# Performance work log

Measured on AMD Instinct MI355X. Metric: run time of the kernel, lower is better.

Reference implementation:

```python
import jax, jax.numpy as jnp
import numpy as np

B, N, DIM = 64, 64, 256
HEADS, P = 4, 16
H, W, C = 56, 56, 256
CH = C // HEADS            # per-head channels = eff_in_dim = eff_out_dim = 64
IN_PTS = HEADS * P         # 64
OUT_PTS = IN_PTS           # 64
TOTAL = CH * CH + IN_PTS * OUT_PTS  # 8192
GRAD_NORM = 1.0 / H

# RestrictGradNorm: identity fwd, clamp grad in bwd
@jax.custom_vjp
def restrict_grad(x):
    return x

def _rg_fwd(x):
    return x, None

def _rg_bwd(_, g):
    return (jnp.clip(g, -GRAD_NORM, GRAD_NORM),)

restrict_grad.defvjp(_rg_fwd, _rg_bwd)


def grid_sample_bilinear(feat, grid):
    # feat [G,c,h,w], grid [G,Hg,Wg,2] in [-1,1]; align_corners=False, zeros padding
    G, c, h, w = feat.shape
    Hg, Wg = grid.shape[1], grid.shape[2]
    Q = Hg * Wg
    x = (grid[..., 0] + 1.0) * 0.5 * w - 0.5
    y = (grid[..., 1] + 1.0) * 0.5 * h - 0.5
    x0f = jnp.floor(x); y0f = jnp.floor(y)
    wx1 = x - x0f; wx0 = 1.0 - wx1
    wy1 = y - y0f; wy0 = 1.0 - wy1
    x0 = x0f.astype(jnp.int32); y0 = y0f.astype(jnp.int32)
    fflat = feat.reshape(G, c, h * w)

    def gather(xi, yi):
        valid = (xi >= 0) & (xi < w) & (yi >= 0) & (yi < h)
        idx = (jnp.clip(yi, 0, h - 1) * w + jnp.clip(xi, 0, w - 1)).reshape(G, Q)
        v = jnp.take_along_axis(fflat, jnp.broadcast_to(idx[:, None, :], (G, c, Q)), axis=2)
        return v * valid.reshape(G, 1, Q)

    out = (gather(x0, y0) * (wx0 * wy0).reshape(G, 1, Q)
           + gather(x0 + 1, y0) * (wx1 * wy0).reshape(G, 1, Q)
           + gather(x0, y0 + 1) * (wx0 * wy1).reshape(G, 1, Q)
           + gather(x0 + 1, y0 + 1) * (wx1 * wy1).reshape(G, 1, Q))
    return out.reshape(G, c, Hg, Wg)


def setup_inputs() -> dict:
    key = jax.random.key(0)
    ks = jax.random.split(key, 10)
    img_feat = jax.random.normal(ks[0], (B, C, H, W), jnp.float32)
    ctr = jax.random.uniform(ks[1], (B, N, 2), jnp.float32) * 0.8 + 0.1
    wh = jax.random.uniform(ks[2], (B, N, 2), jnp.float32) * 0.4 + 0.1
    token_roi = jnp.concatenate([ctr - wh / 2, ctr + wh / 2], axis=-1)
    query = jax.random.normal(ks[3], (B, N, DIM), jnp.float32)
    W_off = jax.random.normal(ks[4], (DIM, HEADS * P * 2), jnp.float32) * 0.02
    b_off = jnp.zeros((HEADS * P * 2,), jnp.float32)
    ln_w = jnp.ones((DIM,), jnp.float32)
    ln_b = jnp.zeros((DIM,), jnp.float32)
    W1 = jax.random.normal(ks[5], (DIM, DIM // 4), jnp.float32) * 0.02
    b1 = jnp.zeros((DIM // 4,), jnp.float32)
    W2 = jax.random.normal(ks[6], (DIM // 4, TOTAL), jnp.float32) * 0.02
    b2 = jax.random.normal(ks[7], (TOTAL,), jnp.float32) * 0.02
    m_beta = jnp.zeros((CH,), jnp.float32)
    s_beta = jnp.zeros((OUT_PTS,), jnp.float32)
    W_out = jax.random.normal(ks[8], (CH * OUT_PTS, DIM), jnp.float32) * 0.02
    b_out = jnp.zeros((DIM,), jnp.float32)
    return dict(img_feat=img_feat, token_roi=token_roi, query=query, W_off=W_off,
                b_off=b_off, ln_w=ln_w, ln_b=ln_b, W1=W1, b1=b1, W2=W2, b2=b2,
                m_beta=m_beta, s_beta=s_beta, W_out=W_out, b_out=b_out)


def _forward(img_feat, token_roi, query, W_off, b_off, ln_w, ln_b, W1, b1, W2, b2,
             m_beta, s_beta, W_out, b_out):
    # 1) sampling offsets from query
    off = (query @ W_off + b_off).reshape(B, N, 1, IN_PTS, 2)
    # 2) make_absolute_sampling_point: normalize over points (unbiased std, as torch)
    mean = off.mean(axis=-2, keepdims=True)
    std = jnp.std(off, axis=-2, ddof=1, keepdims=True) + 1e-7
    off = (off - mean) / (3.0 * std)
    roi_xy = (token_roi[:, :, 2:] + token_roi[:, :, :2]) * 0.5   # [B,N,2]
    roi_wh = token_roi[:, :, 2:] - token_roi[:, :, :2]
    pts = roi_xy[:, :, None, None, :] + off * roi_wh[:, :, None, None, :]  # [B,N,1,HP,2]
    # 3) sampling_from_img_feat: per-head bilinear grid sample
    sp = pts.reshape(B, N, 1, HEADS, P, 2).transpose(0, 3, 1, 2, 4, 5)
    sp = sp.reshape(B * HEADS, N, P, 2)
    sp = restrict_grad(sp)
    grid = sp * 2.0 - 1.0
    feat = img_feat.reshape(B * HEADS, CH, H, W)
    out = grid_sample_bilinear(feat, grid)                        # [B*HEADS, CH, N, P]
    out = out.reshape(B, HEADS, CH, N, 1, P).transpose(0, 3, 4, 1, 5, 2)
    sampled = out.reshape(B * N, IN_PTS, CH)                      # g==1 in AdaptiveMixing
    # 4) AdaptiveMixing: parameter generator (LN eps 1e-6 -> Linear -> Linear)
    mu = query.mean(-1, keepdims=True)
    var = query.var(-1, keepdims=True)
    qn = (query - mu) / jnp.sqrt(var + 1e-6) * ln_w + ln_b
    params = ((qn @ W1 + b1) @ W2 + b2).reshape(B * N, TOTAL)
    cm = params[:, :CH * CH].reshape(B * N, CH, CH)               # channel mixing
    sm = params[:, CH * CH:].reshape(B * N, OUT_PTS, IN_PTS)      # spatial mixing
    x = jax.nn.gelu(jnp.einsum('bpc,bcd->bpd', sampled, cm) + m_beta, approximate=False)
    x = jax.nn.gelu(jnp.einsum('bop,bpc->boc', sm, x) + s_beta[None, :, None], approximate=False)
    x = x.reshape(B, N, OUT_PTS * CH) @ W_out + b_out
    return x


def reference(img_feat, token_roi, query, W_off, b_off, ln_w, ln_b, W1, b1, W2, b2,
              m_beta, s_beta, W_out, b_out):
    return _forward(img_feat, token_roi, query, W_off, b_off, ln_w, ln_b, W1, b1,
                    W2, b2, m_beta, s_beta, W_out, b_out)
```

## Files before the change

### kernel.cpp

```cpp
#include <hip/hip_runtime.h>


typedef unsigned short u16;
typedef u16 u16x8 __attribute__((ext_vector_type(8)));
typedef short bf16x8 __attribute__((ext_vector_type(8)));
typedef float f32x4 __attribute__((ext_vector_type(4)));
#define SA 72
#define MFMA(a, b, c) __builtin_amdgcn_mfma_f32_16x16x32_bf16(a, b, c, 0, 0, 0)

static __device__ __forceinline__ float bf2f(u16 s) {
    union { float f; unsigned u; } v; v.u = ((unsigned)s) << 16; return v.f;
}
static __device__ __forceinline__ u16 f2bf(float f) {
    union { float f; unsigned u; } v; v.f = f;
    unsigned r = v.u + 0x7fffu + ((v.u >> 16) & 1u);
    return (u16)(r >> 16);
}
static __device__ __forceinline__ float gelu(float x) {
    return 0.5f * x * (1.0f + erff(x * 0.70710678118654752f));
}
static __device__ __forceinline__ float loadf(const void* p, size_t i, int isbf) {
    return isbf ? bf2f(((const u16*)p)[i]) : ((const float*)p)[i];
}

__global__ void kdetect(const void* __restrict__ lnw, int* __restrict__ flag) {
    if (threadIdx.x == 0) {
        unsigned v = *(const unsigned*)lnw;
        *flag = (v == 0x3F800000u) ? 0 : 1;
    }
}

__global__ void k0_transpose(const void* __restrict__ img, u16* __restrict__ featT,
                             const int* __restrict__ flag) {
    __shared__ __align__(16) float tile[64 * 65];
    const int pos0 = blockIdx.x * 64, c0 = blockIdx.y * 64, bz = blockIdx.z;
    const int tid = threadIdx.x;
    const int isbf = *flag;
#pragma unroll
    for (int i = 0; i < 16; i++) {
        int e = i * 256 + tid;
        int cy = e >> 6, px = e & 63;
        tile[cy * 65 + px] = loadf(img, ((size_t)bz * 256 + c0 + cy) * 3136 + pos0 + px, isbf);
    }
    __syncthreads();
#pragma unroll
    for (int i = 0; i < 16; i++) {
        int e = i * 256 + tid;
        int cy = e & 63, px = e >> 6;
        featT[((size_t)bz * 3136 + pos0 + px) * 256 + c0 + cy] = f2bf(tile[cy * 65 + px]);
    }
}

__global__ void k1_points(const void* __restrict__ query, const void* __restrict__ roi,
                          const void* __restrict__ W_off, const void* __restrict__ b_off,
                          const void* __restrict__ ln_w, const void* __restrict__ ln_b,
                          const void* __restrict__ W1, const void* __restrict__ b1,
                          const int* __restrict__ flag,
                          float* __restrict__ pts, u16* __restrict__ hbuf) {
    __shared__ float qf[256], qn[256], offl[128], red[4], stats[8];
    const int t = blockIdx.x, tid = threadIdx.x;
    const int isbf = *flag;
    float q = loadf(query, (size_t)t * 256 + tid, isbf);
    qf[tid] = q;
    float v = q;
#pragma unroll
    for (int o = 32; o; o >>= 1) v += __shfl_down(v, o, 64);
    if ((tid & 63) == 0) red[tid >> 6] = v;
    __syncthreads();
    if (tid == 0) stats[0] = (red[0] + red[1] + red[2] + red[3]) * (1.f / 256.f);
    __syncthreads();
    float mu = stats[0];
    float dv = q - mu;
    v = dv * dv;
#pragma unroll
    for (int o = 32; o; o >>= 1) v += __shfl_down(v, o, 64);
    if ((tid & 63) == 0) red[tid >> 6] = v;
    __syncthreads();
    if (tid == 0) stats[1] = (red[0] + red[1] + red[2] + red[3]) * (1.f / 256.f);
    __syncthreads();
    float inv = rsqrtf(stats[1] + 1e-6f);
    qn[tid] = dv * inv * loadf(ln_w, tid, isbf) + loadf(ln_b, tid, isbf);
    __syncthreads();
    if (tid < 128) {
        float a = loadf(b_off, tid, isbf);
        for (int d = 0; d < 256; d++) a = fmaf(qf[d], loadf(W_off, (size_t)d * 128 + tid, isbf), a);
        offl[tid] = a;
    } else if (tid < 192) {
        int k = tid - 128;
        float a = loadf(b1, k, isbf);
        for (int d = 0; d < 256; d++) a = fmaf(qn[d], loadf(W1, (size_t)d * 64 + k, isbf), a);
        hbuf[(size_t)t * 64 + k] = f2bf(a);
    }
    __syncthreads();
    if (tid < 2) {
        float m = 0.f;
        for (int p = 0; p < 64; p++) m += offl[p * 2 + tid];
        m *= (1.f / 64.f);
        float s2 = 0.f;
        for (int p = 0; p < 64; p++) { float d = offl[p * 2 + tid] - m; s2 += d * d; }
        float sd = sqrtf(s2 * (1.f / 63.f));
        stats[2 + tid] = m;
        stats[4 + tid] = 1.f / (3.f * (sd + 1e-7f));
    }
    __syncthreads();
    if (tid < 128) {
        int xy = tid & 1;
        float lo = loadf(roi, (size_t)t * 4 + xy, isbf);
        float hi = loadf(roi, (size_t)t * 4 + 2 + xy, isbf);
        float ctr = 0.5f * (lo + hi), wh = hi - lo;
        pts[(size_t)t * 128 + tid] = ctr + (offl[tid] - stats[2 + xy]) * stats[4 + xy] * wh;
    }
}

__global__ void k2_sample_t(const u16* __restrict__ featT, const float* __restrict__ pts,
                            u16* __restrict__ sampled) {
    const int t = blockIdx.x, tid = threadIdx.x;
    const int pt = tid >> 2, cg = tid & 3;
    const int b = t >> 6, hh = pt >> 4;
    const float px = pts[(size_t)t * 128 + pt * 2], py = pts[(size_t)t * 128 + pt * 2 + 1];
    const float x = px * 56.f - 0.5f, y = py * 56.f - 0.5f;
    const float x0f = floorf(x), y0f = floorf(y);
    const int ix0 = (int)x0f, iy0 = (int)y0f;
    const float wx1 = x - x0f, wx0 = 1.f - wx1, wy1 = y - y0f, wy0 = 1.f - wy1;
    float acc[16];
#pragma unroll
    for (int i = 0; i < 16; i++) acc[i] = 0.f;
    const int chbase = hh * 64 + cg * 16;
#pragma unroll
    for (int corner = 0; corner < 4; corner++) {
        const int xi = ix0 + (corner & 1), yi = iy0 + (corner >> 1);
        const float wgt = ((corner & 1) ? wx1 : wx0) * ((corner >> 1) ? wy1 : wy0);
        if (xi >= 0 && xi < 56 && yi >= 0 && yi < 56) {
            const u16x8* p8 = (const u16x8*)&featT[((size_t)b * 3136 + yi * 56 + xi) * 256 + chbase];
            u16x8 a = p8[0], c = p8[1];
#pragma unroll
            for (int i = 0; i < 8; i++) {
                acc[i]     = fmaf(wgt, bf2f(a[i]), acc[i]);
                acc[8 + i] = fmaf(wgt, bf2f(c[i]), acc[8 + i]);
            }
        }
    }
    u16x8 o0, o1;
#pragma unroll
    for (int i = 0; i < 8; i++) { o0[i] = f2bf(acc[i]); o1[i] = f2bf(acc[8 + i]); }
    u16x8* q8 = (u16x8*)&sampled[(size_t)t * 4096 + pt * 64 + cg * 16];
    q8[0] = o0; q8[1] = o1;
}

__global__ void k2_sample_d(const void* __restrict__ img, const float* __restrict__ pts,
                            u16* __restrict__ sampled, const int* __restrict__ flag) {
    const int t = blockIdx.x, tid = threadIdx.x;
    const int pt = tid >> 2, cg = tid & 3;
    const int b = t >> 6, hh = pt >> 4;
    const int isbf = *flag;
    const float px = pts[(size_t)t * 128 + pt * 2], py = pts[(size_t)t * 128 + pt * 2 + 1];
    const float x = px * 56.f - 0.5f, y = py * 56.f - 0.5f;
    const float x0f = floorf(x), y0f = floorf(y);
    const int ix0 = (int)x0f, iy0 = (int)y0f;
    const float wx1 = x - x0f, wx0 = 1.f - wx1, wy1 = y - y0f, wy0 = 1.f - wy1;
    float acc[16];
#pragma unroll
    for (int i = 0; i < 16; i++) acc[i] = 0.f;
    const int chbase = b * 256 + hh * 64 + cg * 16;
#pragma unroll
    for (int corner = 0; corner < 4; corner++) {
        const int xi = ix0 + (corner & 1), yi = iy0 + (corner >> 1);
        const float wgt = ((corner & 1) ? wx1 : wx0) * ((corner >> 1) ? wy1 : wy0);
        if (xi >= 0 && xi < 56 && yi >= 0 && yi < 56) {
            const size_t sp = yi * 56 + xi;
#pragma unroll
            for (int i = 0; i < 16; i++)
                acc[i] = fmaf(wgt, loadf(img, ((size_t)(chbase + i)) * 3136 + sp, isbf), acc[i]);
        }
    }
    for (int i = 0; i < 16; i++)
        sampled[(size_t)t * 4096 + pt * 64 + cg * 16 + i] = f2bf(acc[i]);
}

__global__ __launch_bounds__(256) void k4_mfma(const u16* __restrict__ hb,
        const void* __restrict__ W2, const void* __restrict__ b2,
        const int* __restrict__ flag, u16* __restrict__ params) {
    __shared__ u16 As[64 * SA];
    __shared__ u16 Bs[64 * SA];
    const int tid = threadIdx.x;
    const int m0 = blockIdx.x * 64, n0 = blockIdx.y * 64;
    const int isbf = *flag;
    const int lane = tid & 63, w = tid >> 6;
    const int wm = w & 1, wn = w >> 1;
    const int l16 = lane & 15, quad = lane >> 4;
    {
        const int row = tid >> 2, kp = (tid & 3) * 16;
        const u16x8* ga = (const u16x8*)&hb[(size_t)(m0 + row) * 64 + kp];
        *(u16x8*)&As[row * SA + kp]     = ga[0];
        *(u16x8*)&As[row * SA + kp + 8] = ga[1];
    }
    {
        const int n = tid & 63, kp = (tid >> 6) * 16;
        u16x8 b0, b1;
#pragma unroll
        for (int j = 0; j < 8; j++) {
            b0[j] = f2bf(loadf(W2, (size_t)(kp + j) * 8192 + n0 + n, isbf));
            b1[j] = f2bf(loadf(W2, (size_t)(kp + 8 + j) * 8192 + n0 + n, isbf));
        }
        *(u16x8*)&Bs[n * SA + kp]     = b0;
        *(u16x8*)&Bs[n * SA + kp + 8] = b1;
    }
    __syncthreads();
    f32x4 acc[2][2];
#pragma unroll
    for (int i = 0; i < 2; i++)
#pragma unroll
        for (int j = 0; j < 2; j++) acc[i][j] = (f32x4){0.f, 0.f, 0.f, 0.f};
#pragma unroll
    for (int kk = 0; kk < 64; kk += 32) {
        bf16x8 af[2], bf[2];
        af[0] = *(const bf16x8*)&As[(wm * 32 + l16) * SA + kk + quad * 8];
        af[1] = *(const bf16x8*)&As[(wm * 32 + 16 + l16) * SA + kk + quad * 8];
        bf[0] = *(const bf16x8*)&Bs[(wn * 32 + l16) * SA + kk + quad * 8];
        bf[1] = *(const bf16x8*)&Bs[(wn * 32 + 16 + l16) * SA + kk + quad * 8];
#pragma unroll
        for (int tm = 0; tm < 2; tm++)
#pragma unroll
            for (int tn = 0; tn < 2; tn++)
                acc[tm][tn] = MFMA(af[tm], bf[tn], acc[tm][tn]);
    }
    float bb[2];
    bb[0] = loadf(b2, n0 + wn * 32 + l16, isbf);
    bb[1] = loadf(b2, n0 + wn * 32 + 16 + l16, isbf);
#pragma unroll
    for (int tm = 0; tm < 2; tm++)
#pragma unroll
        for (int tn = 0; tn < 2; tn++)
#pragma unroll
            for (int r = 0; r < 4; r++) {
                int row = m0 + wm * 32 + tm * 16 + quad * 4 + r;
                int col = n0 + wn * 32 + tn * 16 + l16;
                params[(size_t)row * 8192 + col] = f2bf(acc[tm][tn][r] + bb[tn]);
            }
}

__global__ __launch_bounds__(256) void k5_mfma(const u16* __restrict__ params,
        const void* __restrict__ m_beta, const void* __restrict__ s_beta,
        const int* __restrict__ flag, u16* __restrict__ sampled) {
    __shared__ u16 S[64 * SA];
    __shared__ u16 CMT[64 * SA];
    __shared__ u16 SM[64 * SA];
    __shared__ u16 X1T[64 * SA];
    const int t = blockIdx.x, tid = threadIdx.x;
    const int isbf = *flag;
    const size_t pbase = (size_t)t * 8192, sbase = (size_t)t * 4096;
    const int lane = tid & 63, w = tid >> 6;
    const int wm = w & 1, wn = w >> 1;
    const int l16 = lane & 15, quad = lane >> 4;
    {
        const int r = tid >> 2, cp = (tid & 3) * 16;
        const u16x8* gs = (const u16x8*)&sampled[sbase + r * 64 + cp];
        *(u16x8*)&S[r * SA + cp]     = gs[0];
        *(u16x8*)&S[r * SA + cp + 8] = gs[1];
        const u16x8* gm = (const u16x8*)&params[pbase + 4096 + r * 64 + cp];
        *(u16x8*)&SM[r * SA + cp]     = gm[0];
        *(u16x8*)&SM[r * SA + cp + 8] = gm[1];
    }
    {
        const int d = tid & 63, cp = (tid >> 6) * 16;
        u16x8 b0, b1;
#pragma unroll
        for (int j = 0; j < 8; j++) {
            b0[j] = params[pbase + (size_t)(cp + j) * 64 + d];
            b1[j] = params[pbase + (size_t)(cp + 8 + j) * 64 + d];
        }
        *(u16x8*)&CMT[d * SA + cp]     = b0;
        *(u16x8*)&CMT[d * SA + cp + 8] = b1;
    }
    __syncthreads();
    f32x4 acc[2][2];
#pragma unroll
    for (int i = 0; i < 2; i++)
#pragma unroll
        for (int j = 0; j < 2; j++) acc[i][j] = (f32x4){0.f, 0.f, 0.f, 0.f};
#pragma unroll
    for (int kk = 0; kk < 64; kk += 32) {
        bf16x8 af[2], bf[2];
        af[0] = *(const bf16x8*)&S[(wm * 32 + l16) * SA + kk + quad * 8];
        af[1] = *(const bf16x8*)&S[(wm * 32 + 16 + l16) * SA + kk + quad * 8];
        bf[0] = *(const bf16x8*)&CMT[(wn * 32 + l16) * SA + kk + quad * 8];
        bf[1] = *(const bf16x8*)&CMT[(wn * 32 + 16 + l16) * SA + kk + quad * 8];
#pragma unroll
        for (int tm = 0; tm < 2; tm++)
#pragma unroll
            for (int tn = 0; tn < 2; tn++)
                acc[tm][tn] = MFMA(af[tm], bf[tn], acc[tm][tn]);
    }
    float mb[2];
    mb[0] = loadf(m_beta, wn * 32 + l16, isbf);
    mb[1] = loadf(m_beta, wn * 32 + 16 + l16, isbf);
#pragma unroll
    for (int tm = 0; tm < 2; tm++)
#pragma unroll
        for (int tn = 0; tn < 2; tn++)
#pragma unroll
            for (int r = 0; r < 4; r++) {
                int p = wm * 32 + tm * 16 + quad * 4 + r;
                int d = wn * 32 + tn * 16 + l16;
                X1T[d * SA + p] = f2bf(gelu(acc[tm][tn][r] + mb[tn]));
            }
    __syncthreads();
#pragma unroll
    for (int i = 0; i < 2; i++)
#pragma unroll
        for (int j = 0; j < 2; j++) acc[i][j] = (f32x4){0.f, 0.f, 0.f, 0.f};
#pragma unroll
    for (int kk = 0; kk < 64; kk += 32) {
        bf16x8 af[2], bf[2];
        af[0] = *(const bf16x8*)&SM[(wm * 32 + l16) * SA + kk + quad * 8];
        af[1] = *(const bf16x8*)&SM[(wm * 32 + 16 + l16) * SA + kk + quad * 8];
        bf[0] = *(const bf16x8*)&X1T[(wn * 32 + l16) * SA + kk + quad * 8];
        bf[1] = *(const bf16x8*)&X1T[(wn * 32 + 16 + l16) * SA + kk + quad * 8];
#pragma unroll
        for (int tm = 0; tm < 2; tm++)
#pragma unroll
            for (int tn = 0; tn < 2; tn++)
                acc[tm][tn] = MFMA(af[tm], bf[tn], acc[tm][tn]);
    }
#pragma unroll
    for (int tm = 0; tm < 2; tm++)
#pragma unroll
        for (int tn = 0; tn < 2; tn++)
#pragma unroll
            for (int r = 0; r < 4; r++) {
                int o = wm * 32 + tm * 16 + quad * 4 + r;
                int d = wn * 32 + tn * 16 + l16;
                float sb = loadf(s_beta, o, isbf);
                sampled[sbase + o * 64 + d] = f2bf(gelu(acc[tm][tn][r] + sb));
            }
}

__global__ __launch_bounds__(256) void k6_mfma(const u16* __restrict__ x2b,
        const void* __restrict__ W_out, const void* __restrict__ b_out,
        const int* __restrict__ flag, float* __restrict__ out) {
    __shared__ u16 As[64 * SA];
    __shared__ u16 Bs[64 * SA];
    const int tid = threadIdx.x;
    const int m0 = blockIdx.x * 64, n0 = blockIdx.y * 64;
    const int isbf = *flag;
    const int lane = tid & 63, w = tid >> 6;
    const int wm = w & 1, wn = w >> 1;
    const int l16 = lane & 15, quad = lane >> 4;
    const int sArow = tid >> 2, sAk = (tid & 3) * 16;
    const int sBn = tid & 63, sBk = (tid >> 6) * 16;
    f32x4 acc[2][2];
#pragma unroll
    for (int i = 0; i < 2; i++)
#pragma unroll
        for (int j = 0; j < 2; j++) acc[i][j] = (f32x4){0.f, 0.f, 0.f, 0.f};
    for (int k0 = 0; k0 < 4096; k0 += 64) {
        const u16x8* ga = (const u16x8*)&x2b[(size_t)(m0 + sArow) * 4096 + k0 + sAk];
        u16x8 a0 = ga[0], a1 = ga[1];
        u16x8 b0, b1;
#pragma unroll
        for (int j = 0; j < 8; j++) {
            b0[j] = f2bf(loadf(W_out, (size_t)(k0 + sBk + j) * 256 + n0 + sBn, isbf));
            b1[j] = f2bf(loadf(W_out, (size_t)(k0 + sBk + 8 + j) * 256 + n0 + sBn, isbf));
        }
        __syncthreads();
        *(u16x8*)&As[sArow * SA + sAk]     = a0;
        *(u16x8*)&As[sArow * SA + sAk + 8] = a1;
        *(u16x8*)&Bs[sBn * SA + sBk]       = b0;
        *(u16x8*)&Bs[sBn * SA + sBk + 8]   = b1;
        __syncthreads();
#pragma unroll
        for (int kk = 0; kk < 64; kk += 32) {
            bf16x8 af[2], bf[2];
            af[0] = *(const bf16x8*)&As[(wm * 32 + l16) * SA + kk + quad * 8];
            af[1] = *(const bf16x8*)&As[(wm * 32 + 16 + l16) * SA + kk + quad * 8];
            bf[0] = *(const bf16x8*)&Bs[(wn * 32 + l16) * SA + kk + quad * 8];
            bf[1] = *(const bf16x8*)&Bs[(wn * 32 + 16 + l16) * SA + kk + quad * 8];
#pragma unroll
            for (int tm = 0; tm < 2; tm++)
#pragma unroll
                for (int tn = 0; tn < 2; tn++)
                    acc[tm][tn] = MFMA(af[tm], bf[tn], acc[tm][tn]);
        }
    }
    float bo[2];
    bo[0] = loadf(b_out, n0 + wn * 32 + l16, isbf);
    bo[1] = loadf(b_out, n0 + wn * 32 + 16 + l16, isbf);
#pragma unroll
    for (int tm = 0; tm < 2; tm++)
#pragma unroll
        for (int tn = 0; tn < 2; tn++)
#pragma unroll
            for (int r = 0; r < 4; r++) {
                int row = m0 + wm * 32 + tm * 16 + quad * 4 + r;
                int col = n0 + wn * 32 + tn * 16 + l16;
                out[(size_t)row * 256 + col] = acc[tm][tn][r] + bo[tn];
            }
}

extern "C" void kernel_launch(void* const* d_in, const int* in_sizes, int n_in,
                              void* d_out, int out_size, void* d_ws, size_t ws_size,
                              hipStream_t stream) {
    const void* img    = d_in[0];
    const void* roi    = d_in[1];
    const void* query  = d_in[2];
    const void* W_off  = d_in[3];
    const void* b_off  = d_in[4];
    const void* ln_w   = d_in[5];
    const void* ln_b   = d_in[6];
    const void* W1     = d_in[7];
    const void* b1     = d_in[8];
    const void* W2     = d_in[9];
    const void* b2     = d_in[10];
    const void* m_beta = d_in[11];
    const void* s_beta = d_in[12];
    const void* W_out  = d_in[13];
    const void* b_out  = d_in[14];

    char* ws = (char*)d_ws;
    int*   flag    = (int*)(ws + 0);
    float* pts     = (float*)(ws + 1024);
    u16*   hbuf    = (u16*)(ws + 2098176);
    u16*   sampled = (u16*)(ws + 2622464);
    u16*   params  = (u16*)(ws + 36176896);
    u16*   featT   = (u16*)(ws + 103285760);
    const bool tierA = ws_size >= (size_t)206046208;

    kdetect<<<1, 64, 0, stream>>>(ln_w, flag);
    k1_points<<<4096, 256, 0, stream>>>(query, roi, W_off, b_off, ln_w, ln_b, W1, b1,
                                        flag, pts, hbuf);
    if (tierA) {
        k0_transpose<<<dim3(49, 4, 64), 256, 0, stream>>>(img, featT, flag);
        k2_sample_t<<<4096, 256, 0, stream>>>(featT, pts, sampled);
    } else {
        k2_sample_d<<<4096, 256, 0, stream>>>(img, pts, sampled, flag);
    }
    k4_mfma<<<dim3(64, 128), 256, 0, stream>>>(hbuf, W2, b2, flag, params);
    k5_mfma<<<4096, 256, 0, stream>>>(params, m_beta, s_beta, flag, sampled);
    k6_mfma<<<dim3(64, 4), 256, 0, stream>>>(sampled, W_out, b_out, flag, (float*)d_out);
}
```

Baseline: 588.9 us.

## Pre-transpose weights to bf16 and split-K the output projection

Adds a transpose kernel that converts W2 and W_out once per call into K-contiguous bf16 copies. The param-generator and output GEMMs can then load B tiles with vector loads instead of strided scalar loads with per-element conversion. The output GEMM is also split along K into two halves to double the block count (256 to 512). The halves go to an fp32 partial buffer, and a new reduce kernel sums them and adds the bias. This costs two extra launches, extra workspace and an extra partial-sum round-trip through memory.

```diff
diff --git a/kernel.cpp b/kernel.cpp
--- a/kernel.cpp
+++ b/kernel.cpp
@@ -27,6 +27,27 @@
     if (threadIdx.x == 0) {
         unsigned v = *(const unsigned*)lnw;
         *flag = (v == 0x3F800000u) ? 0 : 1;
+    }
+}
+
+__global__ void ktrans_bf(const void* __restrict__ src, u16* __restrict__ dst,
+                          int R, int C, const int* __restrict__ flag) {
+    __shared__ __align__(16) float tile[64 * 65];
+    const int c0 = blockIdx.x * 64, r0 = blockIdx.y * 64;
+    const int tid = threadIdx.x;
+    const int isbf = *flag;
+#pragma unroll
+    for (int i = 0; i < 16; i++) {
+        int e = i * 256 + tid;
+        int rr = e >> 6, cc = e & 63;
+        tile[rr * 65 + cc] = loadf(src, (size_t)(r0 + rr) * C + c0 + cc, isbf);
+    }
+    __syncthreads();
+#pragma unroll
+    for (int i = 0; i < 16; i++) {
+        int e = i * 256 + tid;
+        int cc = e >> 6, rr = e & 63;
+        dst[(size_t)(c0 + cc) * R + r0 + rr] = f2bf(tile[rr * 65 + cc]);
     }
 }
 
@@ -178,7 +199,7 @@
 }
 
 __global__ __launch_bounds__(256) void k4_mfma(const u16* __restrict__ hb,
-        const void* __restrict__ W2, const void* __restrict__ b2,
+        const u16* __restrict__ W2T, const void* __restrict__ b2,
         const int* __restrict__ flag, u16* __restrict__ params) {
     __shared__ u16 As[64 * SA];
     __shared__ u16 Bs[64 * SA];
@@ -193,17 +214,9 @@
         const u16x8* ga = (const u16x8*)&hb[(size_t)(m0 + row) * 64 + kp];
         *(u16x8*)&As[row * SA + kp]     = ga[0];
         *(u16x8*)&As[row * SA + kp + 8] = ga[1];
-    }
-    {
-        const int n = tid & 63, kp = (tid >> 6) * 16;
-        u16x8 b0, b1;
-#pragma unroll
-        for (int j = 0; j < 8; j++) {
-            b0[j] = f2bf(loadf(W2, (size_t)(kp + j) * 8192 + n0 + n, isbf));
-            b1[j] = f2bf(loadf(W2, (size_t)(kp + 8 + j) * 8192 + n0 + n, isbf));
-        }
-        *(u16x8*)&Bs[n * SA + kp]     = b0;
-        *(u16x8*)&Bs[n * SA + kp + 8] = b1;
+        const u16x8* gb = (const u16x8*)&W2T[(size_t)(n0 + row) * 64 + kp];
+        *(u16x8*)&Bs[row * SA + kp]     = gb[0];
+        *(u16x8*)&Bs[row * SA + kp + 8] = gb[1];
     }
     __syncthreads();
     f32x4 acc[2][2];
@@ -213,16 +226,16 @@
         for (int j = 0; j < 2; j++) acc[i][j] = (f32x4){0.f, 0.f, 0.f, 0.f};
 #pragma unroll
     for (int kk = 0; kk < 64; kk += 32) {
-        bf16x8 af[2], bf[2];
-        af[0] = *(const bf16x8*)&As[(wm * 32 + l16) * SA + kk + quad * 8];
-        af[1] = *(const bf16x8*)&As[(wm * 32 + 16 + l16) * SA + kk + quad * 8];
-        bf[0] = *(const bf16x8*)&Bs[(wn * 32 + l16) * SA + kk + quad * 8];
-        bf[1] = *(const bf16x8*)&Bs[(wn * 32 + 16 + l16) * SA + kk + quad * 8];
+        bf16x8 af[2], bfr[2];
+        af[0]  = *(const bf16x8*)&As[(wm * 32 + l16) * SA + kk + quad * 8];
+        af[1]  = *(const bf16x8*)&As[(wm * 32 + 16 + l16) * SA + kk + quad * 8];
+        bfr[0] = *(const bf16x8*)&Bs[(wn * 32 + l16) * SA + kk + quad * 8];
+        bfr[1] = *(const bf16x8*)&Bs[(wn * 32 + 16 + l16) * SA + kk + quad * 8];
 #pragma unroll
         for (int tm = 0; tm < 2; tm++)
 #pragma unroll
             for (int tn = 0; tn < 2; tn++)
-                acc[tm][tn] = MFMA(af[tm], bf[tn], acc[tm][tn]);
+                acc[tm][tn] = MFMA(af[tm], bfr[tn], acc[tm][tn]);
     }
     float bb[2];
     bb[0] = loadf(b2, n0 + wn * 32 + l16, isbf);
@@ -280,16 +293,16 @@
         for (int j = 0; j < 2; j++) acc[i][j] = (f32x4){0.f, 0.f, 0.f, 0.f};
 #pragma unroll
     for (int kk = 0; kk < 64; kk += 32) {
-        bf16x8 af[2], bf[2];
-        af[0] = *(const bf16x8*)&S[(wm * 32 + l16) * SA + kk + quad * 8];
-        af[1] = *(const bf16x8*)&S[(wm * 32 + 16 + l16) * SA + kk + quad * 8];
-        bf[0] = *(const bf16x8*)&CMT[(wn * 32 + l16) * SA + kk + quad * 8];
-        bf[1] = *(const bf16x8*)&CMT[(wn * 32 + 16 + l16) * SA + kk + quad * 8];
+        bf16x8 af[2], bfr[2];
+        af[0]  = *(const bf16x8*)&S[(wm * 32 + l16) * SA + kk + quad * 8];
+        af[1]  = *(const bf16x8*)&S[(wm * 32 + 16 + l16) * SA + kk + quad * 8];
+        bfr[0] = *(const bf16x8*)&CMT[(wn * 32 + l16) * SA + kk + quad * 8];
+        bfr[1] = *(const bf16x8*)&CMT[(wn * 32 + 16 + l16) * SA + kk + quad * 8];
 #pragma unroll
         for (int tm = 0; tm < 2; tm++)
 #pragma unroll
             for (int tn = 0; tn < 2; tn++)
-                acc[tm][tn] = MFMA(af[tm], bf[tn], acc[tm][tn]);
+                acc[tm][tn] = MFMA(af[tm], bfr[tn], acc[tm][tn]);
     }
     float mb[2];
     mb[0] = loadf(m_beta, wn * 32 + l16, isbf);
@@ -311,16 +324,16 @@
         for (int j = 0; j < 2; j++) acc[i][j] = (f32x4){0.f, 0.f, 0.f, 0.f};
 #pragma unroll
     for (int kk = 0; kk < 64; kk += 32) {
-        bf16x8 af[2], bf[2];
-        af[0] = *(const bf16x8*)&SM[(wm * 32 + l16) * SA + kk + quad * 8];
-        af[1] = *(const bf16x8*)&SM[(wm * 32 + 16 + l16) * SA + kk + quad * 8];
-        bf[0] = *(const bf16x8*)&X1T[(wn * 32 + l16) * SA + kk + quad * 8];
-        bf[1] = *(const bf16x8*)&X1T[(wn * 32 + 16 + l16) * SA + kk + quad * 8];
+        bf16x8 af[2], bfr[2];
+        af[0]  = *(const bf16x8*)&SM[(wm * 32 + l16) * SA + kk + quad * 8];
+        af[1]  = *(const bf16x8*)&SM[(wm * 32 + 16 + l16) * SA + kk + quad * 8];
+        bfr[0] = *(const bf16x8*)&X1T[(wn * 32 + l16) * SA + kk + quad * 8];
+        bfr[1] = *(const bf16x8*)&X1T[(wn * 32 + 16 + l16) * SA + kk + quad * 8];
 #pragma unroll
         for (int tm = 0; tm < 2; tm++)
 #pragma unroll
             for (int tn = 0; tn < 2; tn++)
-                acc[tm][tn] = MFMA(af[tm], bf[tn], acc[tm][tn]);
+                acc[tm][tn] = MFMA(af[tm], bfr[tn], acc[tm][tn]);
     }
 #pragma unroll
     for (int tm = 0; tm < 2; tm++)
@@ -336,55 +349,47 @@
 }
 
 __global__ __launch_bounds__(256) void k6_mfma(const u16* __restrict__ x2b,
-        const void* __restrict__ W_out, const void* __restrict__ b_out,
-        const int* __restrict__ flag, float* __restrict__ out) {
+        const u16* __restrict__ WoutT, float* __restrict__ part) {
     __shared__ u16 As[64 * SA];
     __shared__ u16 Bs[64 * SA];
     const int tid = threadIdx.x;
-    const int m0 = blockIdx.x * 64, n0 = blockIdx.y * 64;
-    const int isbf = *flag;
+    const int m0 = blockIdx.x * 64, n0 = blockIdx.y * 64, kz = blockIdx.z;
     const int lane = tid & 63, w = tid >> 6;
     const int wm = w & 1, wn = w >> 1;
     const int l16 = lane & 15, quad = lane >> 4;
-    const int sArow = tid >> 2, sAk = (tid & 3) * 16;
-    const int sBn = tid & 63, sBk = (tid >> 6) * 16;
+    const int sRow = tid >> 2, sK = (tid & 3) * 16;
     f32x4 acc[2][2];
 #pragma unroll
     for (int i = 0; i < 2; i++)
 #pragma unroll
         for (int j = 0; j < 2; j++) acc[i][j] = (f32x4){0.f, 0.f, 0.f, 0.f};
-    for (int k0 = 0; k0 < 4096; k0 += 64) {
-        const u16x8* ga = (const u16x8*)&x2b[(size_t)(m0 + sArow) * 4096 + k0 + sAk];
+    const int kbeg = kz * 2048, kend = kbeg + 2048;
+    for (int k0 = kbeg; k0 < kend; k0 += 64) {
+        const u16x8* ga = (const u16x8*)&x2b[(size_t)(m0 + sRow) * 4096 + k0 + sK];
         u16x8 a0 = ga[0], a1 = ga[1];
-        u16x8 b0, b1;
-#pragma unroll
-        for (int j = 0; j < 8; j++) {
-            b0[j] = f2bf(loadf(W_out, (size_t)(k0 + sBk + j) * 256 + n0 + sBn, isbf));
-            b1[j] = f2bf(loadf(W_out, (size_t)(k0 + sBk + 8 + j) * 256 + n0 + sBn, isbf));
+        const u16x8* gb = (const u16x8*)&WoutT[(size_t)(n0 + sRow) * 4096 + k0 + sK];
+        u16x8 b0 = gb[0], b1 = gb[1];
+        __syncthreads();
+        *(u16x8*)&As[sRow * SA + sK]     = a0;
+        *(u16x8*)&As[sRow * SA + sK + 8] = a1;
+        *(u16x8*)&Bs[sRow * SA + sK]     = b0;
+        *(u16x8*)&Bs[sRow * SA + sK + 8] = b1;
+        __syncthreads();
+#pragma unroll
+        for (int kk = 0; kk < 64; kk += 32) {
+            bf16x8 af[2], bfr[2];
+            af[0]  = *(const bf16x8*)&As[(wm * 32 + l16) * SA + kk + quad * 8];
+            af[1]  = *(const bf16x8*)&As[(wm * 32 + 16 + l16) * SA + kk + quad * 8];
+            bfr[0] = *(const bf16x8*)&Bs[(wn * 32 + l16) * SA + kk + quad * 8];
+            bfr[1] = *(const bf16x8*)&Bs[(wn * 32 + 16 + l16) * SA + kk + quad * 8];
+#pragma unroll
+            for (int tm = 0; tm < 2; tm++)
+#pragma unroll
+                for (int tn = 0; tn < 2; tn++)
+                    acc[tm][tn] = MFMA(af[tm], bfr[tn], acc[tm][tn]);
         }
-        __syncthreads();
-        *(u16x8*)&As[sArow * SA + sAk]     = a0;
-        *(u16x8*)&As[sArow * SA + sAk + 8] = a1;
-        *(u16x8*)&Bs[sBn * SA + sBk]       = b0;
-        *(u16x8*)&Bs[sBn * SA + sBk + 8]   = b1;
-        __syncthreads();
-#pragma unroll
-        for (int kk = 0; kk < 64; kk += 32) {
-            bf16x8 af[2], bf[2];
-            af[0] = *(const bf16x8*)&As[(wm * 32 + l16) * SA + kk + quad * 8];
-            af[1] = *(const bf16x8*)&As[(wm * 32 + 16 + l16) * SA + kk + quad * 8];
-            bf[0] = *(const bf16x8*)&Bs[(wn * 32 + l16) * SA + kk + quad * 8];
-            bf[1] = *(const bf16x8*)&Bs[(wn * 32 + 16 + l16) * SA + kk + quad * 8];
-#pragma unroll
-            for (int tm = 0; tm < 2; tm++)
-#pragma unroll
-                for (int tn = 0; tn < 2; tn++)
-                    acc[tm][tn] = MFMA(af[tm], bf[tn], acc[tm][tn]);
-        }
-    }
-    float bo[2];
-    bo[0] = loadf(b_out, n0 + wn * 32 + l16, isbf);
-    bo[1] = loadf(b_out, n0 + wn * 32 + 16 + l16, isbf);
+    }
+    float* pbase = part + (size_t)kz * (4096 * 256);
 #pragma unroll
     for (int tm = 0; tm < 2; tm++)
 #pragma unroll
@@ -393,8 +398,15 @@
             for (int r = 0; r < 4; r++) {
                 int row = m0 + wm * 32 + tm * 16 + quad * 4 + r;
                 int col = n0 + wn * 32 + tn * 16 + l16;
-                out[(size_t)row * 256 + col] = acc[tm][tn][r] + bo[tn];
+                pbase[(size_t)row * 256 + col] = acc[tm][tn][r];
             }
+}
+
+__global__ void k7_reduce(const float* __restrict__ part, const void* __restrict__ b_out,
+                          const int* __restrict__ flag, float* __restrict__ out) {
+    const int i = blockIdx.x * 256 + threadIdx.x;
+    const int isbf = *flag;
+    out[i] = part[i] + part[4096 * 256 + i] + loadf(b_out, i & 255, isbf);
 }
 
 extern "C" void kernel_launch(void* const* d_in, const int* in_sizes, int n_in,
@@ -422,19 +434,25 @@
     u16*   hbuf    = (u16*)(ws + 2098176);
     u16*   sampled = (u16*)(ws + 2622464);
     u16*   params  = (u16*)(ws + 36176896);
-    u16*   featT   = (u16*)(ws + 103285760);
-    const bool tierA = ws_size >= (size_t)206046208;
+    u16*   W2T     = (u16*)(ws + 103285760);
+    u16*   WoutT   = (u16*)(ws + 104334336);
+    float* part    = (float*)(ws + 106431488);
+    u16*   featT   = (u16*)(ws + 114820096);
+    const bool tierA = ws_size >= (size_t)217580544;
 
     kdetect<<<1, 64, 0, stream>>>(ln_w, flag);
     k1_points<<<4096, 256, 0, stream>>>(query, roi, W_off, b_off, ln_w, ln_b, W1, b1,
                                         flag, pts, hbuf);
+    ktrans_bf<<<dim3(128, 1), 256, 0, stream>>>(W2, W2T, 64, 8192, flag);
+    ktrans_bf<<<dim3(4, 64), 256, 0, stream>>>(W_out, WoutT, 4096, 256, flag);
     if (tierA) {
         k0_transpose<<<dim3(49, 4, 64), 256, 0, stream>>>(img, featT, flag);
         k2_sample_t<<<4096, 256, 0, stream>>>(featT, pts, sampled);
     } else {
         k2_sample_d<<<4096, 256, 0, stream>>>(img, pts, sampled, flag);
     }
-    k4_mfma<<<dim3(64, 128), 256, 0, stream>>>(hbuf, W2, b2, flag, params);
+    k4_mfma<<<dim3(64, 128), 256, 0, stream>>>(hbuf, W2T, b2, flag, params);
     k5_mfma<<<4096, 256, 0, stream>>>(params, m_beta, s_beta, flag, sampled);
-    k6_mfma<<<dim3(64, 4), 256, 0, stream>>>(sampled, W_out, b_out, flag, (float*)d_out);
-}
+    k6_mfma<<<dim3(64, 4, 2), 256, 0, stream>>>(sampled, WoutT, part);
+    k7_reduce<<<4096, 256, 0, stream>>>(part, b_out, flag, (float*)d_out);
+}
```

Result: faster. 551.2 us (-6.4%).
